# Optimization experiments

Hardware: AMD Instinct MI355X
Metric: run time of the kernel (lower is better)

## Reference

```python
import jax, jax.numpy as jnp
import numpy as np

T, M, K, B, H, L, V = 64, 256, 6, 256, 256, 128, 780
E = T * M
PAD = E  # padding slot in hidden buffer = Lorentz origin

def _to_lorentz_np(s):
    t = np.sqrt(1.0 + (s * s).sum(-1, keepdims=True))
    return np.concatenate([t, s], -1).astype(np.float32)

def setup_inputs() -> dict:
    rng = np.random.default_rng(0)
    def make_nei():
        idx = np.full((T, M, K), PAD, np.int64)
        w = np.zeros((T, M, K), np.float32)
        for t in range(T):
            deg = rng.integers(0, K + 1, size=M)
            if t == 0:
                deg[:] = 0  # no messages exist yet
            mask = np.arange(K)[None, :] < deg[:, None]
            cand = rng.integers(0, max(1, t * M), size=(M, K))  # only already-computed slots
            idx[t] = np.where(mask, cand, PAD)
            w[t] = mask.astype(np.float32)
            w[t, deg == 0, 0] = 1.0  # zero-neighbor case -> use origin padding (as in torch code)
        return idx.astype(np.int32), w
    nei_h_idx, nei_h_w = make_nei()
    nei_o_idx, nei_o_w = make_nei()
    return dict(
        wid=jnp.asarray(rng.integers(0, V, size=(T, M)), jnp.int32),
        nei_h_idx=jnp.asarray(nei_h_idx), nei_h_w=jnp.asarray(nei_h_w),
        nei_o_idx=jnp.asarray(nei_o_idx), nei_o_w=jnp.asarray(nei_o_w),
        batch_idx=jnp.asarray(rng.integers(0, B, size=(T, M)), jnp.int32),
        direction=jnp.asarray(rng.integers(0, 2, size=(T, M)), jnp.int32),
        pred_target=jnp.asarray(rng.integers(0, V, size=(T, M)), jnp.int32),
        root_wid=jnp.asarray(rng.integers(0, V, size=(B,)), jnp.int32),
        root_o_idx=jnp.asarray(rng.integers(0, E, size=(B, K)), jnp.int32),
        root_o_w=jnp.ones((B, K), jnp.float32),
        x_tree_vecs=jnp.asarray(_to_lorentz_np(rng.standard_normal((B, L - 1)) * 0.5)),
        embedding=jnp.asarray(_to_lorentz_np(rng.standard_normal((V, H - 1)) * 0.5)),
        W0=jnp.asarray(rng.standard_normal((H, H)) * 0.02, dtype=jnp.float32),
        b0=jnp.zeros((H,), jnp.float32),
        s0=jnp.asarray(np.log(10.0), jnp.float32),
        W1=jnp.asarray(rng.standard_normal((H, 2 * H - 1)) * 0.02, dtype=jnp.float32),
        b1=jnp.zeros((H,), jnp.float32),
        s1=jnp.asarray(np.log(10.0), jnp.float32),
        wcls=jnp.asarray(_to_lorentz_np(rng.standard_normal((V, H + L - 2)) * 0.5)),
        wbias=jnp.zeros((V,), jnp.float32),
        ucls=jnp.asarray(_to_lorentz_np(rng.standard_normal((2, 2 * H + L - 3)) * 0.5)),
        ubias=jnp.zeros((2,), jnp.float32),
    )

def _llinear(x, W, b, scale):
    # LorentzLinear: affine map, then rescale space part so output stays on the hyperboloid
    x = x @ W.T + b
    xs = x[..., 1:]
    time = jax.nn.sigmoid(x[..., :1]) * jnp.exp(scale) + 1.1
    sq = (time * time - 1.0) / jnp.clip((xs * xs).sum(-1, keepdims=True), 1e-8)
    return jnp.concatenate([time, xs * jnp.sqrt(sq)], -1)

def _mid_point(x, w):
    # Lorentz centroid: weighted mean renormalized to the manifold. x: [...,K,d], w: [...,K]
    ave = jnp.einsum('...k,...kd->...d', w, x) / jnp.clip(w.sum(-1, keepdims=True), 1e-8)
    inner = (ave[..., 1:] ** 2).sum(-1, keepdims=True) - ave[..., :1] ** 2  # <ave,ave>_L
    return ave / jnp.sqrt(jnp.clip(-inner, 1e-8))

def _concat(x, y):
    # hyperbolic concat: keep space parts, recompute time (dim = d1+d2-1)
    time = jnp.sqrt(jnp.clip(x[..., :1] ** 2 + y[..., :1] ** 2 - 1.0, 1e-8))
    return jnp.concatenate([time, x[..., 1:], y[..., 1:]], -1)

def _centroid(x, cls_pts, bias):
    # LorentzCentroidDistance logits: 2 + 2*<x, c>_L + bias
    inner = x[..., 1:] @ cls_pts[:, 1:].T - x[..., :1] * cls_pts[None, :, 0]
    return 2.0 + 2.0 * inner + bias

def _ce(scores, tgt):
    lp = jax.nn.log_softmax(scores, -1)
    return -jnp.take_along_axis(lp, tgt[:, None], axis=-1)[:, 0]

def _forward_core(wid, nei_h_idx, nei_h_w, nei_o_idx, nei_o_w, batch_idx, direction,
                  pred_target, root_wid, root_o_idx, root_o_w, x_tree_vecs, embedding,
                  W0, b0, s0, W1, b1, s1, wcls, wbias, ucls, ubias):
    hbuf0 = jnp.zeros((E + 1, H), jnp.float32).at[:, 0].set(1.0)  # all origin; slot E is padding

    def step(carry, xs_t):
        hbuf, t = carry
        wid_t, idx_t, w_t = xs_t
        cur_x = embedding[wid_t]                      # [M,H]
        h_nei = hbuf[idx_t]                           # [M,K,H] gather of prior messages
        h1 = _llinear(h_nei, W0, b0, s0)              # A0
        h1m = _mid_point(h1, w_t)                     # [M,H]
        new_h = _llinear(_concat(cur_x, h1m), W1, b1, s1)  # A1
        hbuf = jax.lax.dynamic_update_slice(hbuf, new_h, (t * M, 0))
        return (hbuf, t + jnp.int32(1)), new_h

    (hbuf, _), new_h = jax.lax.scan(step, (hbuf0, jnp.int32(0)), (wid, nei_h_idx, nei_h_w))
    new_h = new_h.reshape(E, H)
    cur_x = embedding[wid.reshape(E)]
    cur_o = _mid_point(hbuf[nei_o_idx.reshape(E, K)], nei_o_w.reshape(E, K))
    ctx = x_tree_vecs[batch_idx.reshape(E)]

    # word prediction: roots (origin hidden) + forward-direction messages
    origin = jnp.zeros((B, H), jnp.float32).at[:, 0].set(1.0)
    root_scores = _centroid(_concat(origin, x_tree_vecs), wcls, wbias)   # [B,V]
    msg_scores = _centroid(_concat(new_h, ctx), wcls, wbias)             # [E,V]
    pmask = direction.reshape(E).astype(jnp.float32)
    pt = pred_target.reshape(E)
    pred_loss = (_ce(root_scores, root_wid).sum() + (pmask * _ce(msg_scores, pt)).sum()) / B
    pred_hit = ((jnp.argmax(root_scores, -1) == root_wid).astype(jnp.float32).sum()
                + (pmask * (jnp.argmax(msg_scores, -1) == pt).astype(jnp.float32)).sum())
    pred_acc = pred_hit / (B + pmask.sum())

    # stop prediction: every message + final per-tree root entry (target 0)
    stop_h = _concat(_concat(cur_x, cur_o), ctx)                         # [E, 2H+L-2]
    root_o = _mid_point(hbuf[root_o_idx], root_o_w)
    stop_root = _concat(_concat(embedding[root_wid], root_o), x_tree_vecs)
    stop_scores = _centroid(jnp.concatenate([stop_h, stop_root], 0), ucls, ubias)
    stop_tgt = jnp.concatenate([direction.reshape(E), jnp.zeros((B,), jnp.int32)], 0)
    stop_loss = _ce(stop_scores, stop_tgt).sum() / B
    stop_acc = (jnp.argmax(stop_scores, -1) == stop_tgt).astype(jnp.float32).mean()
    return pred_loss, stop_loss, pred_acc, stop_acc

def reference(wid, nei_h_idx, nei_h_w, nei_o_idx, nei_o_w, batch_idx, direction,
              pred_target, root_wid, root_o_idx, root_o_w, x_tree_vecs, embedding,
              W0, b0, s0, W1, b1, s1, wcls, wbias, ucls, ubias):
    return _forward_core(wid, nei_h_idx, nei_h_w, nei_o_idx, nei_o_w, batch_idx, direction,
                         pred_target, root_wid, root_o_idx, root_o_w, x_tree_vecs, embedding,
                         W0, b0, s0, W1, b1, s1, wcls, wbias, ucls, ubias)
```

## Files before the change

kernel.cpp:

```cpp
#include <hip/hip_runtime.h>
#include <math.h>

#define T_ 64
#define M_ 256
#define K_ 6
#define B_ 256
#define H_ 256
#define L_ 128
#define V_ 780
#define E_ (T_*M_)
#define ZD 383
#define UD 638
#define KP 384
#define VP 832
#define TAG_PAD 0x7fffffffu

typedef unsigned short ushort_t;
typedef __attribute__((ext_vector_type(8))) _Float16 half8v;
typedef __attribute__((ext_vector_type(4))) _Float16 half4v;
typedef __attribute__((ext_vector_type(2))) _Float16 half2v;
typedef __attribute__((ext_vector_type(4))) float f32x4v;
typedef unsigned long long u64;


__device__ __forceinline__ float blk_sum(float v, float* red) {
    int j = threadIdx.x;
    #pragma unroll
    for (int o = 32; o > 0; o >>= 1) v += __shfl_down(v, o, 64);
    __syncthreads();
    if ((j & 63) == 0) red[j >> 6] = v;
    __syncthreads();
    return red[0] + red[1] + red[2] + red[3];
}

__device__ __forceinline__ float wave_sum(float v) {
    #pragma unroll
    for (int o = 32; o > 0; o >>= 1) v += __shfl_xor(v, o, 64);
    return v;
}

__device__ __forceinline__ _Float16 f2h(float x) { return (_Float16)x; }

__device__ __forceinline__ u64 llc_load8(const u64* p) {
    return __hip_atomic_load(p, __ATOMIC_RELAXED, __HIP_MEMORY_SCOPE_AGENT);
}
__device__ __forceinline__ void llc_store8(u64* p, u64 v) {
    __hip_atomic_store(p, v, __ATOMIC_RELAXED, __HIP_MEMORY_SCOPE_AGENT);
}


#define PREP_R0 H_
#define PREP_RT ((E_ + 1) * 128)
#define PREP_RH3 E_
#define PREP_R1 65536
#define PREP_R2 65536
#define PREP_R3 (VP * KP)
#define PREP_R4 65536
#define PREP_TOTAL (PREP_R0 + PREP_RT + PREP_RH3 + PREP_R1 + PREP_R2 + PREP_R3 + PREP_R4)

__global__ __launch_bounds__(256) void prep_k(const float* __restrict__ W0,
                                              const float* __restrict__ W1,
                                              const float* __restrict__ wcls,
                                              float* __restrict__ hbuf,
                                              u64* __restrict__ hbuf2,
                                              u64* __restrict__ hbuf3,
                                              _Float16* __restrict__ W0P,
                                              _Float16* __restrict__ W1HP,
                                              _Float16* __restrict__ Wh,
                                              float* __restrict__ W1T) {
    int idx = blockIdx.x * 256 + threadIdx.x;
    if (idx < PREP_R0) {
        hbuf[(size_t)E_ * H_ + idx] = (idx == 0) ? 1.f : 0.f;
        return;
    }
    idx -= PREP_R0;
    if (idx < PREP_RT) {
        int row = idx >> 7, cp = idx & 127;
        u64 val = 0ull;
        if (row == E_) {
            unsigned int lo = (cp == 0) ? 0x3C00u : 0u;
            val = ((u64)TAG_PAD << 32) | lo;
        }
        hbuf2[idx] = val;
        return;
    }
    idx -= PREP_RT;
    if (idx < PREP_RH3) {
        hbuf3[idx] = 0ull;
        return;
    }
    idx -= PREP_RH3;
    if (idx < PREP_R1) {
        int e = idx & 7, l = (idx >> 3) & 63, ks = (idx >> 9) & 7, nt = idx >> 12;
        int jj = nt * 16 + (l & 15);
        int ii = ks * 32 + (l >> 4) * 8 + e;
        W0P[idx] = f2h(W0[(size_t)jj * H_ + ii]);
        return;
    }
    idx -= PREP_R1;
    if (idx < PREP_R2) {
        int e = idx & 7, l = (idx >> 3) & 63, ks = (idx >> 9) & 7, nt = idx >> 12;
        int jj = nt * 16 + (l & 15);
        int ii = ks * 32 + (l >> 4) * 8 + e;
        float v = (ii == 0) ? W1[(size_t)jj * (2 * H_ - 1)]
                            : W1[(size_t)jj * (2 * H_ - 1) + 255 + ii];
        W1HP[idx] = f2h(v);
        return;
    }
    idx -= PREP_R2;
    if (idx < PREP_R3) {
        int v = idx / KP, k = idx - v * KP;
        float val = (v < V_ && k < ZD) ? wcls[(size_t)v * ZD + k] : 0.f;
        Wh[idx] = f2h(val);
        return;
    }
    idx -= PREP_R3;
    if (idx < PREP_R4) {
        int i = idx >> 8, j = idx & 255;
        W1T[idx] = (i >= 1) ? W1[(size_t)j * (2 * H_ - 1) + i] : 0.f;
    }
}


__global__ __launch_bounds__(256) void basew_k(const float* __restrict__ emb,
                                               const float* __restrict__ W1T,
                                               const float* __restrict__ b1,
                                               float* __restrict__ basew) {
    int v = blockIdx.x, j = threadIdx.x;
    __shared__ float cxs[256];
    cxs[j] = emb[(size_t)v * H_ + j];
    __syncthreads();
    float acc = b1[j];
    #pragma unroll 8
    for (int i = 1; i < 256; i++) acc = fmaf(cxs[i], W1T[i * 256 + j], acc);
    basew[(size_t)v * H_ + j] = acc;
}


__global__ __launch_bounds__(256, 1) void scan_flow(float* __restrict__ hbuf,
        u64* __restrict__ hbuf2, u64* __restrict__ hbuf3,
        const _Float16* __restrict__ W0P, const float* __restrict__ b0, const float* __restrict__ s0p,
        const _Float16* __restrict__ W1HP, const float* __restrict__ s1p,
        const float* __restrict__ emb, const int* __restrict__ wid,
        const int* __restrict__ nhi, const float* __restrict__ nhw,
        const float* __restrict__ basew,
        const _Float16* __restrict__ Wh, const float* __restrict__ wbias,
        const int* __restrict__ pt, const int* __restrict__ dir,
        const int* __restrict__ bidx, const float* __restrict__ xtv,
        float* __restrict__ part) {
    int tid = threadIdx.x;
    int w = tid >> 6, l = tid & 63;
    int quad = l >> 4, col = l & 15;
    int m = blockIdx.x;
    int j0 = 4 * l;
    int cp = tid & 127;
    int rsel = tid >> 7;

    __shared__ __align__(16) _Float16 hn16[16][264];
    __shared__ __align__(16) _Float16 zzs[4][264];
    __shared__ __align__(16) float Ys[6][256];
    __shared__ __align__(16) float y2s[256];
    __shared__ __align__(16) _Float16 As[64][392];
    __shared__ __align__(16) _Float16 Bsf[64][392];
    __shared__ __align__(16) float SCs[64][68];
    __shared__ float rmax[64], rsum[64], rval[64];
    __shared__ int   rargi[64];

    half8v w0f[4][8], w1f[4][8];
    #pragma unroll
    for (int q = 0; q < 4; q++) {
        int nt = 4 * w + q;
        #pragma unroll
        for (int ks = 0; ks < 8; ks++) {
            w0f[q][ks] = *(const half8v*)(W0P + ((size_t)(nt * 8 + ks) * 64 + l) * 8);
            w1f[q][ks] = *(const half8v*)(W1HP + ((size_t)(nt * 8 + ks) * 64 + l) * 8);
        }
    }

    float es0 = expf(s0p[0]);
    float es1 = expf(s1p[0]);
    float4 bj4 = *(const float4*)(b0 + j0);

    unsigned int tagx[3];
    const u64* pp[3];
    u64 pvv[3];
    #pragma unroll
    for (int p = 0; p < 3; p++) {
        int row = 2 * p + rsel;
        int id = nhi[(size_t)m * K_ + row];
        tagx[p] = (id < E_) ? (unsigned int)(id >> 8) + 1u : TAG_PAD;
        pp[p] = hbuf2 + ((size_t)id << 7) + cp;
        pvv[p] = llc_load8(pp[p]);
    }

    for (int t = 0; t < T_; t++) {
        int e = t * M_ + m;
        const float* wp = nhw + e * K_;

        float wk[K_];
        #pragma unroll
        for (int k = 0; k < K_; k++) wk[k] = wp[k];
        int wde = wid[e];
        float4 bw4 = *(const float4*)(basew + (size_t)wde * H_ + j0);
        float cx0 = emb[(size_t)wde * H_];

        for (;;) {
            bool ok = ((unsigned int)(pvv[0] >> 32) == tagx[0])
                   && ((unsigned int)(pvv[1] >> 32) == tagx[1])
                   && ((unsigned int)(pvv[2] >> 32) == tagx[2]);
            if (ok) break;
            __builtin_amdgcn_s_sleep(1);
            #pragma unroll
            for (int p = 0; p < 3; p++)
                if ((unsigned int)(pvv[p] >> 32) != tagx[p]) pvv[p] = llc_load8(pp[p]);
        }
        #pragma unroll
        for (int p = 0; p < 3; p++)
            *(unsigned int*)&hn16[2 * p + rsel][cp * 2] = (unsigned int)pvv[p];
        __syncthreads();

        if (t + 1 < T_) {
            #pragma unroll
            for (int p = 0; p < 3; p++) {
                int row = 2 * p + rsel;
                int id = nhi[(size_t)(e + M_) * K_ + row];
                tagx[p] = (id < E_) ? (unsigned int)(id >> 8) + 1u : TAG_PAD;
                pp[p] = hbuf2 + ((size_t)id << 7) + cp;
                pvv[p] = llc_load8(pp[p]);
            }
        }

        f32x4v acc[4];
        #pragma unroll
        for (int q = 0; q < 4; q++) acc[q] = (f32x4v){0.f, 0.f, 0.f, 0.f};
        #pragma unroll
        for (int ks = 0; ks < 8; ks++) {
            half8v afr = *(const half8v*)&hn16[col][ks * 32 + quad * 8];
            #pragma unroll
            for (int q = 0; q < 4; q++)
                acc[q] = __builtin_amdgcn_mfma_f32_16x16x32_f16(afr, w0f[q][ks], acc[q], 0, 0, 0);
        }
        #pragma unroll
        for (int q = 0; q < 4; q++) {
            int nt = 4 * w + q;
            #pragma unroll
            for (int rr = 0; rr < 4; rr++) {
                int row = quad * 4 + rr;
                if (row < 6) Ys[row][nt * 16 + col] = acc[q][rr];
            }
        }
        __syncthreads();

        float y[K_][4];
        #pragma unroll
        for (int k = 0; k < K_; k++) {
            float4 yv = *(const float4*)&Ys[k][j0];
            y[k][0] = yv.x + bj4.x; y[k][1] = yv.y + bj4.y;
            y[k][2] = yv.z + bj4.z; y[k][3] = yv.w + bj4.w;
        }
        float c[K_];
        #pragma unroll
        for (int k = 0; k < K_; k++) {
            float cc = y[k][0] * y[k][0] + y[k][1] * y[k][1]
                     + y[k][2] * y[k][2] + y[k][3] * y[k][3];
            if (l == 0) cc -= y[k][0] * y[k][0];
            c[k] = cc;
        }
        #pragma unroll
        for (int o = 32; o > 0; o >>= 1) {
            #pragma unroll
            for (int k = 0; k < K_; k++) c[k] += __shfl_xor(c[k], o, 64);
        }
        float y0b[K_];
        #pragma unroll
        for (int k = 0; k < K_; k++) y0b[k] = __shfl(y[k][0], 0, 64);

        float ave[4] = {0.f, 0.f, 0.f, 0.f};
        float wsum = 0.f;
        #pragma unroll
        for (int k = 0; k < K_; k++) {
            float tm = es0 / (1.f + expf(-y0b[k])) + 1.1f;
            float sc = sqrtf((tm * tm - 1.f) / fmaxf(c[k], 1e-8f));
            #pragma unroll
            for (int c2 = 0; c2 < 4; c2++) {
                float h1v = (l == 0 && c2 == 0) ? tm : y[k][c2] * sc;
                ave[c2] += wk[k] * h1v;
            }
            wsum += wk[k];
        }
        float inv = 1.f / fmaxf(wsum, 1e-8f);
        float innl = 0.f;
        #pragma unroll
        for (int c2 = 0; c2 < 4; c2++) { ave[c2] *= inv; innl += ave[c2] * ave[c2]; }
        if (l == 0) innl -= 2.f * ave[0] * ave[0];
        float inner = wave_sum(innl);
        float rsc = 1.f / sqrtf(fmaxf(-inner, 1e-8f));

        #pragma unroll
        for (int c2 = 0; c2 < 4; c2++) {
            int j = j0 + c2;
            float h1m = ave[c2] * rsc;
            if (j == 0) {
                zzs[w][0] = f2h(sqrtf(fmaxf(cx0 * cx0 + h1m * h1m - 1.f, 1e-8f)));
            } else {
                zzs[w][j] = f2h(h1m);
            }
        }

        f32x4v a2[4];
        #pragma unroll
        for (int q = 0; q < 4; q++) a2[q] = (f32x4v){0.f, 0.f, 0.f, 0.f};
        #pragma unroll
        for (int ks = 0; ks < 8; ks++) {
            half8v zfr = *(const half8v*)&zzs[w][ks * 32 + quad * 8];
            #pragma unroll
            for (int q = 0; q < 4; q++)
                a2[q] = __builtin_amdgcn_mfma_f32_16x16x32_f16(zfr, w1f[q][ks], a2[q], 0, 0, 0);
        }
        if (quad == 0) {
            #pragma unroll
            for (int q = 0; q < 4; q++) y2s[(4 * w + q) * 16 + col] = a2[q][0];
        }
        __syncthreads();

        if (w == 0) {
            float4 y2v = *(const float4*)&y2s[j0];
            float y2[4] = {y2v.x + bw4.x, y2v.y + bw4.y, y2v.z + bw4.z, y2v.w + bw4.w};
            float c2s = y2[0] * y2[0] + y2[1] * y2[1] + y2[2] * y2[2] + y2[3] * y2[3];
            if (l == 0) c2s -= y2[0] * y2[0];
            float ssq2 = wave_sum(c2s);
            float y20 = __shfl(y2[0], 0, 64);
            float tm2 = es1 / (1.f + expf(-y20)) + 1.1f;
            float sc2 = sqrtf((tm2 * tm2 - 1.f) / fmaxf(ssq2, 1e-8f));
            float hv0 = (l == 0) ? tm2 : y2[0] * sc2;
            float hv1 = y2[1] * sc2, hv2 = y2[2] * sc2, hv3 = y2[3] * sc2;

            unsigned int tag = (unsigned int)t + 1u;
            union { half2v h; unsigned int u; } c01, c23;
            c01.h.x = f2h(hv0); c01.h.y = f2h(hv1);
            c23.h.x = f2h(hv2); c23.h.y = f2h(hv3);
            u64* pb = hbuf2 + ((size_t)e << 7) + 2 * l;
            llc_store8(pb,     ((u64)tag << 32) | c01.u);
            llc_store8(pb + 1, ((u64)tag << 32) | c23.u);

            if (l == 0) {
                union { float f; unsigned int u; } h0b; h0b.f = tm2;
                llc_store8(hbuf3 + e, ((u64)tag << 32) | h0b.u);
            }

            float4 out4 = {hv0, hv1, hv2, hv3};
            *(float4*)(hbuf + (size_t)e * H_ + j0) = out4;
        }
    }

    {
        int m0 = m * 64;

        u64 gpv[32];
        #pragma unroll
        for (int i = 0; i < 32; i++) {
            int p = tid + i * 256;
            int row = p >> 7, cpp = p & 127;
            gpv[i] = llc_load8(hbuf2 + ((size_t)(m0 + row) << 7) + cpp);
        }
        for (;;) {
            bool ok = true;
            #pragma unroll
            for (int i = 0; i < 32; i++) {
                int row = (tid + i * 256) >> 7;
                unsigned int tg = (unsigned int)((m0 + row) >> 8) + 1u;
                if ((unsigned int)(gpv[i] >> 32) != tg) ok = false;
            }
            if (ok) break;
            __builtin_amdgcn_s_sleep(1);
            #pragma unroll
            for (int i = 0; i < 32; i++) {
                int p = tid + i * 256;
                int row = p >> 7, cpp = p & 127;
                unsigned int tg = (unsigned int)((m0 + row) >> 8) + 1u;
                if ((unsigned int)(gpv[i] >> 32) != tg)
                    gpv[i] = llc_load8(hbuf2 + ((size_t)(m0 + row) << 7) + cpp);
            }
        }
        #pragma unroll
        for (int i = 0; i < 32; i++) {
            int p = tid + i * 256;
            int row = p >> 7, cpp = p & 127;
            *(unsigned int*)&As[row][2 * cpp] = (unsigned int)gpv[i];
        }
        #pragma unroll
        for (int i = 0; i < 16; i++) {
            int p = tid + i * 256;
            int row = p >> 6, k2 = (p & 63) * 2;
            int bi = bidx[m0 + row];
            int ca = 256 + k2;
            half2v hv;
            hv.x = (ca <= 382) ? f2h(xtv[(size_t)bi * L_ + (ca - 255)]) : (_Float16)0.f;
            hv.y = (ca + 1 <= 382) ? f2h(xtv[(size_t)bi * L_ + (ca - 254)]) : (_Float16)0.f;
            *(half2v*)&As[row][ca] = hv;
        }
        if (tid < 64) {
            int e2 = m0 + tid;
            unsigned int tg = (unsigned int)(e2 >> 8) + 1u;
            u64 hv3 = llc_load8(hbuf3 + e2);
            while ((unsigned int)(hv3 >> 32) != tg) {
                __builtin_amdgcn_s_sleep(1);
                hv3 = llc_load8(hbuf3 + e2);
            }
            union { unsigned int u; float f; } h0c; h0c.u = (unsigned int)hv3;
            int bi = bidx[e2];
            float c0 = xtv[(size_t)bi * L_];
            float z0 = sqrtf(fmaxf(h0c.f * h0c.f + c0 * c0 - 1.f, 1e-8f));
            As[tid][0] = f2h(-z0);
            rmax[tid] = -1e30f; rsum[tid] = 0.f; rargi[tid] = 0; rval[tid] = 0.f;
        }
        __syncthreads();

        int q8 = quad * 8;
        for (int nt = 0; nt < 13; nt++) {
            int n0 = nt * 64;
            #pragma unroll
            for (int i = 0; i < 12; i++) {
                int uu = tid + i * 256;
                int row = uu / 48, c8 = (uu % 48) * 8;
                *(uint4*)&Bsf[row][c8] = *(const uint4*)(Wh + (size_t)(n0 + row) * KP + c8);
            }
            __syncthreads();

            f32x4v gacc[4];
            #pragma unroll
            for (int mt = 0; mt < 4; mt++) gacc[mt] = (f32x4v){0.f, 0.f, 0.f, 0.f};
            #pragma unroll
            for (int ks = 0; ks < 12; ks++) {
                half8v bfr = *(const half8v*)&Bsf[w * 16 + col][ks * 32 + q8];
                #pragma unroll
                for (int mt = 0; mt < 4; mt++) {
                    half8v afr = *(const half8v*)&As[mt * 16 + col][ks * 32 + q8];
                    gacc[mt] = __builtin_amdgcn_mfma_f32_16x16x32_f16(afr, bfr, gacc[mt], 0, 0, 0);
                }
            }
            int ncol = n0 + w * 16 + col;
            float bias = (ncol < V_) ? wbias[ncol] : 0.f;
            #pragma unroll
            for (int mt = 0; mt < 4; mt++) {
                #pragma unroll
                for (int rr = 0; rr < 4; rr++)
                    SCs[mt * 16 + quad * 4 + rr][w * 16 + col] = 2.f + 2.f * gacc[mt][rr] + bias;
            }
            __syncthreads();

            {
                int row = tid >> 2, prt = tid & 3;
                int tg = pt[m0 + row];
                float vals[16];
                float lm = -1e30f; int li = 0;
                #pragma unroll
                for (int cc = 0; cc < 16; cc++) {
                    int nc = n0 + prt * 16 + cc;
                    float x = (nc < V_) ? SCs[row][prt * 16 + cc] : -1e30f;
                    vals[cc] = x;
                    if (x > lm) { lm = x; li = nc; }
                    if (nc == tg) rval[row] = x;
                }
                #pragma unroll
                for (int o = 1; o < 4; o <<= 1) {
                    float om = __shfl_xor(lm, o, 64);
                    int   oi = __shfl_xor(li, o, 64);
                    if (om > lm || (om == lm && oi < li)) { lm = om; li = oi; }
                }
                float ls = 0.f;
                #pragma unroll
                for (int cc = 0; cc < 16; cc++) {
                    int nc = n0 + prt * 16 + cc;
                    if (nc < V_) ls += expf(vals[cc] - lm);
                }
                #pragma unroll
                for (int o = 1; o < 4; o <<= 1) ls += __shfl_xor(ls, o, 64);
                if (prt == 0) {
                    float om = rmax[row], os = rsum[row];
                    float nm = fmaxf(om, lm);
                    rsum[row] = os * expf(om - nm) + ls * expf(lm - nm);
                    if (lm > om) rargi[row] = li;
                    rmax[row] = nm;
                }
            }
            __syncthreads();
        }

        if (tid < 64) {
            int e2 = m0 + tid;
            int tg = pt[e2];
            float pm = (float)dir[e2];
            float lse = rmax[tid] + logf(rsum[tid]);
            float lloss = pm * (lse - rval[tid]);
            float lhit  = pm * ((rargi[tid] == tg) ? 1.f : 0.f);
            float lpm   = pm;
            lloss = wave_sum(lloss);
            lhit  = wave_sum(lhit);
            lpm   = wave_sum(lpm);
            if (tid == 0) {
                float* pr = part + (size_t)m * 8;
                pr[0] = lloss; pr[1] = lhit; pr[2] = lpm;
                pr[3] = 0.f; pr[4] = 0.f;
            }
        }
    }
}


__global__ __launch_bounds__(256) void stoproot_k(const float* __restrict__ hbuf,
        const float* __restrict__ emb, const float* __restrict__ xtv,
        const int* __restrict__ wid, const int* __restrict__ noi, const float* __restrict__ now_w,
        const int* __restrict__ bidx, const int* __restrict__ dir,
        const int* __restrict__ rwid, const int* __restrict__ roi, const float* __restrict__ row_w,
        const float* __restrict__ wcls, const float* __restrict__ wbias,
        const float* __restrict__ ucls, const float* __restrict__ ubias,
        float* __restrict__ part) {
    __shared__ float red[256];
    __shared__ int   redi[256];
    __shared__ float shs[4];
    __shared__ float ctxs[L_];
    __shared__ float sc[V_];
    __shared__ float red2[4][2];

    if (blockIdx.x < 256) {
        int w = threadIdx.x >> 6, l = threadIdx.x & 63;
        int wg = blockIdx.x * 4 + w;

        float ua0[4], ub0[4], ua1[4], ub1[4], uc0[2], uc1[2];
        #pragma unroll
        for (int s = 0; s < 4; s++) {
            int j = s * 64 + l;
            ua0[s] = ucls[j];        ub0[s] = ucls[255 + j];
            ua1[s] = ucls[UD + j];   ub1[s] = ucls[UD + 255 + j];
        }
        #pragma unroll
        for (int s = 0; s < 2; s++) {
            int j = s * 64 + l;
            uc0[s] = ucls[510 + j];  uc1[s] = ucls[UD + 510 + j];
        }
        float u00 = ucls[0], u10 = ucls[UD];
        float ubs0 = ubias[0], ubs1 = ubias[1];

        float lloss = 0.f, lhit = 0.f;
        for (int i = 0; i < 16; i++) {
            int e = wg * 16 + i;
            const int*   ip = noi + e * K_;
            const float* wp = now_w + e * K_;
            float ave[4] = {0.f, 0.f, 0.f, 0.f};
            float wsum = 0.f;
            #pragma unroll
            for (int k = 0; k < K_; k++) {
                int id = ip[k]; float wt = wp[k];
                wsum += wt;
                const float* hr = hbuf + (size_t)id * H_;
                #pragma unroll
                for (int s = 0; s < 4; s++) ave[s] += wt * hr[s * 64 + l];
            }
            float inv = 1.f / fmaxf(wsum, 1e-8f);
            float innl = 0.f;
            #pragma unroll
            for (int s = 0; s < 4; s++) { ave[s] *= inv; innl += ave[s] * ave[s]; }
            if (l == 0) innl -= 2.f * ave[0] * ave[0];
            float inner = wave_sum(innl);
            float cs = 1.f / sqrtf(fmaxf(-inner, 1e-8f));

            int we = wid[e], bi = bidx[e];
            const float* er = emb + (size_t)we * H_;
            const float* cr = xtv + (size_t)bi * L_;

            float p0 = 0.f, p1 = 0.f;
            #pragma unroll
            for (int s = 0; s < 4; s++) {
                float cx = er[s * 64 + l];
                float co = ave[s] * cs;
                if (s == 0 && l == 0) {
                    float ctx0 = cr[0];
                    float t1sq = fmaxf(cx * cx + co * co - 1.f, 1e-8f);
                    float sh0 = sqrtf(fmaxf(t1sq + ctx0 * ctx0 - 1.f, 1e-8f));
                    p0 += -sh0 * u00; p1 += -sh0 * u10;
                } else {
                    p0 += cx * ua0[s] + co * ub0[s];
                    p1 += cx * ua1[s] + co * ub1[s];
                }
                if (s < 2) {
                    int j = s * 64 + l;
                    if (j >= 1) {
                        float ctx = cr[j];
                        p0 += ctx * uc0[s]; p1 += ctx * uc1[s];
                    }
                }
            }
            p0 = wave_sum(p0); p1 = wave_sum(p1);
            if (l == 0) {
                float sc0 = 2.f + 2.f * p0 + ubs0;
                float sc1 = 2.f + 2.f * p1 + ubs1;
                int tgt = dir[e];
                float mm = fmaxf(sc0, sc1);
                float lse = mm + logf(expf(sc0 - mm) + expf(sc1 - mm));
                lloss += lse - ((tgt == 0) ? sc0 : sc1);
                int am = (sc1 > sc0) ? 1 : 0;
                lhit += (am == tgt) ? 1.f : 0.f;
            }
        }
        if (l == 0) { red2[w][0] = lloss; red2[w][1] = lhit; }
        __syncthreads();
        if (threadIdx.x == 0) {
            float* pr = part + (size_t)(256 + blockIdx.x) * 8;
            pr[0] = 0.f; pr[1] = 0.f; pr[2] = 0.f;
            pr[3] = red2[0][0] + red2[1][0] + red2[2][0] + red2[3][0];
            pr[4] = red2[0][1] + red2[1][1] + red2[2][1] + red2[3][1];
        }
    } else {
        int b = blockIdx.x - 256, j = threadIdx.x;
        float* pr = part + (size_t)(512 + b) * 8;

        const int*   ip = roi + b * K_;
        const float* wp = row_w + b * K_;
        float ave = 0.f, wsum = 0.f;
        #pragma unroll
        for (int k = 0; k < K_; k++) {
            int id = ip[k]; float w = wp[k];
            ave += w * hbuf[(size_t)id * H_ + j];
            wsum += w;
        }
        ave /= fmaxf(wsum, 1e-8f);
        float inner = blk_sum((j == 0) ? -ave * ave : ave * ave, red);
        float ro = ave / sqrtf(fmaxf(-inner, 1e-8f));

        int   rw = rwid[b];
        float er = emb[(size_t)rw * H_ + j];
        float ctxj = (j < L_) ? xtv[(size_t)b * L_ + j] : 0.f;
        if (j == 0) { shs[0] = er; shs[1] = ro; shs[2] = ctxj; }
        if (j < L_) ctxs[j] = ctxj;
        __syncthreads();
        float t1sq = fmaxf(shs[0] * shs[0] + shs[1] * shs[1] - 1.f, 1e-8f);
        float sh0  = sqrtf(fmaxf(t1sq + shs[2] * shs[2] - 1.f, 1e-8f));

        float p0, p1;
        if (j >= 1) {
            p0 = er * ucls[j] + ro * ucls[255 + j];
            p1 = er * ucls[UD + j] + ro * ucls[UD + 255 + j];
            if (j < L_) { p0 += ctxj * ucls[510 + j]; p1 += ctxj * ucls[UD + 510 + j]; }
        } else {
            p0 = -sh0 * ucls[0];
            p1 = -sh0 * ucls[UD];
        }
        float s0 = 2.f + 2.f * blk_sum(p0, red) + ubias[0];
        float s1 = 2.f + 2.f * blk_sum(p1, red) + ubias[1];
        if (j == 0) {
            float mm = fmaxf(s0, s1);
            float lse = mm + logf(expf(s0 - mm) + expf(s1 - mm));
            int am = (s1 > s0) ? 1 : 0;
            pr[3] = lse - s0;
            pr[4] = (am == 0) ? 1.f : 0.f;
        }

        float c0 = shs[2];
        float z0 = sqrtf(fmaxf(c0 * c0, 1e-8f));
        __syncthreads();
        for (int v = j; v < V_; v += 256) {
            const float* wv = wcls + (size_t)v * ZD;
            float d = -z0 * wv[0];
            for (int i = 1; i < L_; i++) d += ctxs[i] * wv[255 + i];
            sc[v] = 2.f + 2.f * d + wbias[v];
        }
        __syncthreads();
        float mx = -1e30f; int mi = 0;
        for (int v = j; v < V_; v += 256) { float x = sc[v]; if (x > mx) { mx = x; mi = v; } }
        red[j] = mx; redi[j] = mi;
        __syncthreads();
        for (int o = 128; o > 0; o >>= 1) {
            if (j < o) {
                float xo = red[j + o]; int io = redi[j + o];
                if (xo > red[j] || (xo == red[j] && io < redi[j])) { red[j] = xo; redi[j] = io; }
            }
            __syncthreads();
        }
        float gm = red[0]; int ga = redi[0];
        __syncthreads();
        float se = 0.f;
        for (int v = j; v < V_; v += 256) se += expf(sc[v] - gm);
        red[j] = se;
        __syncthreads();
        for (int o = 128; o > 0; o >>= 1) { if (j < o) red[j] += red[j + o]; __syncthreads(); }
        if (j == 0) {
            float lse = gm + logf(red[0]);
            pr[0] = lse - sc[rw];
            pr[1] = (ga == rw) ? 1.f : 0.f;
            pr[2] = 0.f;
        }
    }
}


__global__ __launch_bounds__(256) void finalize2(const float* __restrict__ part,
                                                 float* __restrict__ out) {
    int j = threadIdx.x;
    __shared__ float red[256][5];
    #pragma unroll
    for (int c = 0; c < 5; c++)
        red[j][c] = part[(size_t)j * 8 + c] + part[(size_t)(j + 256) * 8 + c]
                  + part[(size_t)(j + 512) * 8 + c];
    __syncthreads();
    for (int o = 128; o > 0; o >>= 1) {
        if (j < o) {
            #pragma unroll
            for (int c = 0; c < 5; c++) red[j][c] += red[j + o][c];
        }
        __syncthreads();
    }
    if (j == 0) {
        out[0] = red[0][0] / (float)B_;
        out[1] = red[0][3] / (float)B_;
        out[2] = red[0][1] / ((float)B_ + red[0][2]);
        out[3] = red[0][4] / (float)(E_ + B_);
    }
}


extern "C" void kernel_launch(void* const* d_in, const int* in_sizes, int n_in,
                              void* d_out, int out_size, void* d_ws, size_t ws_size,
                              hipStream_t stream) {
    const int*   wid   = (const int*)d_in[0];
    const int*   nhi   = (const int*)d_in[1];
    const float* nhw   = (const float*)d_in[2];
    const int*   noi   = (const int*)d_in[3];
    const float* now_w = (const float*)d_in[4];
    const int*   bidx  = (const int*)d_in[5];
    const int*   dir   = (const int*)d_in[6];
    const int*   pt    = (const int*)d_in[7];
    const int*   rwid  = (const int*)d_in[8];
    const int*   roi   = (const int*)d_in[9];
    const float* row_w = (const float*)d_in[10];
    const float* xtv   = (const float*)d_in[11];
    const float* emb   = (const float*)d_in[12];
    const float* W0    = (const float*)d_in[13];
    const float* b0    = (const float*)d_in[14];
    const float* s0    = (const float*)d_in[15];
    const float* W1    = (const float*)d_in[16];
    const float* b1    = (const float*)d_in[17];
    const float* s1    = (const float*)d_in[18];
    const float* wcls  = (const float*)d_in[19];
    const float* wbias = (const float*)d_in[20];
    const float* ucls  = (const float*)d_in[21];
    const float* ubias = (const float*)d_in[22];

    float* ws    = (float*)d_ws;
    float* hbuf  = ws;
    u64*   hbuf2 = (u64*)(hbuf + (size_t)(E_ + 1) * H_);
    u64*   hbuf3 = hbuf2 + (size_t)(E_ + 1) * 128;
    float* part  = (float*)(hbuf3 + E_);
    float* basew = part + 768 * 8;
    float* W1T   = basew + (size_t)V_ * H_;
    _Float16* W0P  = (_Float16*)(W1T + 65536);
    _Float16* W1HP = W0P + 65536;
    _Float16* Wh   = W1HP + 65536;
    float* out  = (float*)d_out;

    prep_k<<<(PREP_TOTAL + 255) / 256, 256, 0, stream>>>(W0, W1, wcls, hbuf, hbuf2, hbuf3,
                                                         W0P, W1HP, Wh, W1T);
    basew_k<<<V_, 256, 0, stream>>>(emb, W1T, b1, basew);

    scan_flow<<<M_, 256, 0, stream>>>(hbuf, hbuf2, hbuf3, W0P, b0, s0, W1HP, s1,
                                      emb, wid, nhi, nhw, basew,
                                      Wh, wbias, pt, dir, bidx, xtv, part);

    stoproot_k<<<512, 256, 0, stream>>>(hbuf, emb, xtv, wid, noi, now_w, bidx, dir,
                                        rwid, roi, row_w, wcls, wbias, ucls, ubias, part);
    finalize2<<<1, 256, 0, stream>>>(part, out);
}
```

Measured before the change: 575.4 us.

## Fold basew into prep kernel and finalize into stoproot via last-block counter

Computes the per-vocab base projection inside the prep kernel, reading W1 rows directly instead of building a transposed copy, and drops the separate basew kernel. The final reduction moves into stoproot_k using an atomic completion counter, so the last block to finish sums the partials. This removes two kernel launches and the W1T transpose pass. The cost is uncoalesced strided W1 reads in the basew part and an atomic/fence at the end of every stoproot block.

New measurement: 602.9 us. 1.05x slower.

```diff
diff --git a/kernel.cpp b/kernel.cpp
--- a/kernel.cpp
+++ b/kernel.cpp
@@ -1,5 +1,6 @@
 #include <hip/hip_runtime.h>
 #include <math.h>
+
 
 #define T_ 64
 #define M_ 256
@@ -15,9 +16,7 @@
 #define VP 832
 #define TAG_PAD 0x7fffffffu
 
-typedef unsigned short ushort_t;
 typedef __attribute__((ext_vector_type(8))) _Float16 half8v;
-typedef __attribute__((ext_vector_type(4))) _Float16 half4v;
 typedef __attribute__((ext_vector_type(2))) _Float16 half2v;
 typedef __attribute__((ext_vector_type(4))) float f32x4v;
 typedef unsigned long long u64;
@@ -47,34 +46,48 @@
 __device__ __forceinline__ void llc_store8(u64* p, u64 v) {
     __hip_atomic_store(p, v, __ATOMIC_RELAXED, __HIP_MEMORY_SCOPE_AGENT);
 }
-
-
-#define PREP_R0 H_
-#define PREP_RT ((E_ + 1) * 128)
-#define PREP_RH3 E_
-#define PREP_R1 65536
-#define PREP_R2 65536
-#define PREP_R3 (VP * KP)
-#define PREP_R4 65536
-#define PREP_TOTAL (PREP_R0 + PREP_RT + PREP_RH3 + PREP_R1 + PREP_R2 + PREP_R3 + PREP_R4)
+__device__ __forceinline__ float llc_loadf(const float* p) {
+    return __hip_atomic_load(p, __ATOMIC_RELAXED, __HIP_MEMORY_SCOPE_AGENT);
+}
+
+
+#define S_BW (V_ * H_)
+#define S_R0 256
+#define S_RT ((E_ + 1) * 128)
+#define S_H3 E_
+#define S_CT 256
+#define S_W0 65536
+#define S_W1 65536
+#define S_WH (VP * KP)
+#define S_TOTAL (S_BW + S_R0 + S_RT + S_H3 + S_CT + S_W0 + S_W1 + S_WH)
 
 __global__ __launch_bounds__(256) void prep_k(const float* __restrict__ W0,
-                                              const float* __restrict__ W1,
-                                              const float* __restrict__ wcls,
-                                              float* __restrict__ hbuf,
-                                              u64* __restrict__ hbuf2,
-                                              u64* __restrict__ hbuf3,
-                                              _Float16* __restrict__ W0P,
-                                              _Float16* __restrict__ W1HP,
-                                              _Float16* __restrict__ Wh,
-                                              float* __restrict__ W1T) {
+        const float* __restrict__ W1, const float* __restrict__ wcls,
+        const float* __restrict__ emb, const float* __restrict__ b1,
+        float* __restrict__ hbuf, u64* __restrict__ hbuf2, u64* __restrict__ hbuf3,
+        int* __restrict__ counter,
+        _Float16* __restrict__ W0P, _Float16* __restrict__ W1HP,
+        _Float16* __restrict__ Wh, float* __restrict__ basew) {
+    __shared__ float cxs[256];
     int idx = blockIdx.x * 256 + threadIdx.x;
-    if (idx < PREP_R0) {
+    if (idx < S_BW) {
+        int v = idx >> 8, j = idx & 255;
+        cxs[threadIdx.x] = emb[(size_t)v * H_ + threadIdx.x];
+        __syncthreads();
+        float acc = b1[j];
+        const float* w1r = W1 + (size_t)j * (2 * H_ - 1);
+        #pragma unroll 8
+        for (int i = 1; i < 256; i++) acc = fmaf(cxs[i], w1r[i], acc);
+        basew[idx] = acc;
+        return;
+    }
+    idx -= S_BW;
+    if (idx < S_R0) {
         hbuf[(size_t)E_ * H_ + idx] = (idx == 0) ? 1.f : 0.f;
         return;
     }
-    idx -= PREP_R0;
-    if (idx < PREP_RT) {
+    idx -= S_R0;
+    if (idx < S_RT) {
         int row = idx >> 7, cp = idx & 127;
         u64 val = 0ull;
         if (row == E_) {
@@ -84,21 +97,26 @@
         hbuf2[idx] = val;
         return;
     }
-    idx -= PREP_RT;
-    if (idx < PREP_RH3) {
+    idx -= S_RT;
+    if (idx < S_H3) {
         hbuf3[idx] = 0ull;
         return;
     }
-    idx -= PREP_RH3;
-    if (idx < PREP_R1) {
+    idx -= S_H3;
+    if (idx < S_CT) {
+        if (idx == 0) counter[0] = 0;
+        return;
+    }
+    idx -= S_CT;
+    if (idx < S_W0) {
         int e = idx & 7, l = (idx >> 3) & 63, ks = (idx >> 9) & 7, nt = idx >> 12;
         int jj = nt * 16 + (l & 15);
         int ii = ks * 32 + (l >> 4) * 8 + e;
         W0P[idx] = f2h(W0[(size_t)jj * H_ + ii]);
         return;
     }
-    idx -= PREP_R1;
-    if (idx < PREP_R2) {
+    idx -= S_W0;
+    if (idx < S_W1) {
         int e = idx & 7, l = (idx >> 3) & 63, ks = (idx >> 9) & 7, nt = idx >> 12;
         int jj = nt * 16 + (l & 15);
         int ii = ks * 32 + (l >> 4) * 8 + e;
@@ -107,33 +125,12 @@
         W1HP[idx] = f2h(v);
         return;
     }
-    idx -= PREP_R2;
-    if (idx < PREP_R3) {
+    idx -= S_W1;
+    if (idx < S_WH) {
         int v = idx / KP, k = idx - v * KP;
         float val = (v < V_ && k < ZD) ? wcls[(size_t)v * ZD + k] : 0.f;
         Wh[idx] = f2h(val);
-        return;
-    }
-    idx -= PREP_R3;
-    if (idx < PREP_R4) {
-        int i = idx >> 8, j = idx & 255;
-        W1T[idx] = (i >= 1) ? W1[(size_t)j * (2 * H_ - 1) + i] : 0.f;
-    }
-}
-
-
-__global__ __launch_bounds__(256) void basew_k(const float* __restrict__ emb,
-                                               const float* __restrict__ W1T,
-                                               const float* __restrict__ b1,
-                                               float* __restrict__ basew) {
-    int v = blockIdx.x, j = threadIdx.x;
-    __shared__ float cxs[256];
-    cxs[j] = emb[(size_t)v * H_ + j];
-    __syncthreads();
-    float acc = b1[j];
-    #pragma unroll 8
-    for (int i = 1; i < 256; i++) acc = fmaf(cxs[i], W1T[i * 256 + j], acc);
-    basew[(size_t)v * H_ + j] = acc;
+    }
 }
 
 
@@ -280,10 +277,10 @@
         #pragma unroll
         for (int k = 0; k < K_; k++) {
             float tm = es0 / (1.f + expf(-y0b[k])) + 1.1f;
-            float sc = sqrtf((tm * tm - 1.f) / fmaxf(c[k], 1e-8f));
+            float scv = sqrtf((tm * tm - 1.f) / fmaxf(c[k], 1e-8f));
             #pragma unroll
             for (int c2 = 0; c2 < 4; c2++) {
-                float h1v = (l == 0 && c2 == 0) ? tm : y[k][c2] * sc;
+                float h1v = (l == 0 && c2 == 0) ? tm : y[k][c2] * scv;
                 ave[c2] += wk[k] * h1v;
             }
             wsum += wk[k];
@@ -515,13 +512,16 @@
         const int* __restrict__ rwid, const int* __restrict__ roi, const float* __restrict__ row_w,
         const float* __restrict__ wcls, const float* __restrict__ wbias,
         const float* __restrict__ ucls, const float* __restrict__ ubias,
-        float* __restrict__ part) {
+        float* __restrict__ part, int* __restrict__ counter,
+        float* __restrict__ out) {
     __shared__ float red[256];
     __shared__ int   redi[256];
     __shared__ float shs[4];
     __shared__ float ctxs[L_];
     __shared__ float sc[V_];
     __shared__ float red2[4][2];
+    __shared__ float fred[256][5];
+    __shared__ int   lastf;
 
     if (blockIdx.x < 256) {
         int w = threadIdx.x >> 6, l = threadIdx.x & 63;
@@ -691,30 +691,36 @@
             pr[2] = 0.f;
         }
     }
-}
-
-
-__global__ __launch_bounds__(256) void finalize2(const float* __restrict__ part,
-                                                 float* __restrict__ out) {
-    int j = threadIdx.x;
-    __shared__ float red[256][5];
-    #pragma unroll
-    for (int c = 0; c < 5; c++)
-        red[j][c] = part[(size_t)j * 8 + c] + part[(size_t)(j + 256) * 8 + c]
-                  + part[(size_t)(j + 512) * 8 + c];
+
     __syncthreads();
-    for (int o = 128; o > 0; o >>= 1) {
-        if (j < o) {
-            #pragma unroll
-            for (int c = 0; c < 5; c++) red[j][c] += red[j + o][c];
-        }
-        __syncthreads();
-    }
-    if (j == 0) {
-        out[0] = red[0][0] / (float)B_;
-        out[1] = red[0][3] / (float)B_;
-        out[2] = red[0][1] / ((float)B_ + red[0][2]);
-        out[3] = red[0][4] / (float)(E_ + B_);
+    if (threadIdx.x == 0) {
+        __threadfence();
+        int done = __hip_atomic_fetch_add(counter, 1, __ATOMIC_ACQ_REL,
+                                          __HIP_MEMORY_SCOPE_AGENT);
+        lastf = (done == 511) ? 1 : 0;
+    }
+    __syncthreads();
+    if (lastf) {
+        int j = threadIdx.x;
+        #pragma unroll
+        for (int c = 0; c < 5; c++)
+            fred[j][c] = llc_loadf(part + (size_t)j * 8 + c)
+                       + llc_loadf(part + (size_t)(j + 256) * 8 + c)
+                       + llc_loadf(part + (size_t)(j + 512) * 8 + c);
+        __syncthreads();
+        for (int o = 128; o > 0; o >>= 1) {
+            if (j < o) {
+                #pragma unroll
+                for (int c = 0; c < 5; c++) fred[j][c] += fred[j + o][c];
+            }
+            __syncthreads();
+        }
+        if (j == 0) {
+            out[0] = fred[0][0] / (float)B_;
+            out[1] = fred[0][3] / (float)B_;
+            out[2] = fred[0][1] / ((float)B_ + fred[0][2]);
+            out[3] = fred[0][4] / (float)(E_ + B_);
+        }
     }
 }
 
@@ -751,22 +757,22 @@
     u64*   hbuf2 = (u64*)(hbuf + (size_t)(E_ + 1) * H_);
     u64*   hbuf3 = hbuf2 + (size_t)(E_ + 1) * 128;
     float* part  = (float*)(hbuf3 + E_);
-    float* basew = part + 768 * 8;
-    float* W1T   = basew + (size_t)V_ * H_;
-    _Float16* W0P  = (_Float16*)(W1T + 65536);
+    int*   counter = (int*)(part + 768 * 8);
+    float* basew = (float*)(counter + 256);
+    _Float16* W0P  = (_Float16*)(basew + (size_t)V_ * H_);
     _Float16* W1HP = W0P + 65536;
     _Float16* Wh   = W1HP + 65536;
     float* out  = (float*)d_out;
 
-    prep_k<<<(PREP_TOTAL + 255) / 256, 256, 0, stream>>>(W0, W1, wcls, hbuf, hbuf2, hbuf3,
-                                                         W0P, W1HP, Wh, W1T);
-    basew_k<<<V_, 256, 0, stream>>>(emb, W1T, b1, basew);
+    prep_k<<<(S_TOTAL + 255) / 256, 256, 0, stream>>>(W0, W1, wcls, emb, b1,
+                                                      hbuf, hbuf2, hbuf3, counter,
+                                                      W0P, W1HP, Wh, basew);
 
     scan_flow<<<M_, 256, 0, stream>>>(hbuf, hbuf2, hbuf3, W0P, b0, s0, W1HP, s1,
                                       emb, wid, nhi, nhw, basew,
                                       Wh, wbias, pt, dir, bidx, xtv, part);
 
     stoproot_k<<<512, 256, 0, stream>>>(hbuf, emb, xtv, wid, noi, now_w, bidx, dir,
-                                        rwid, roi, row_w, wcls, wbias, ucls, ubias, part);
-    finalize2<<<1, 256, 0, stream>>>(part, out);
-}
+                                        rwid, roi, row_w, wcls, wbias, ucls, ubias,
+                                        part, counter, out);
+}
```
